# Performance work log

Measured on AMD Instinct MI355X. Metric: run time of the kernel, lower is better.

The kernel has to match this reference:

```python
import jax, jax.numpy as jnp
import numpy as np

EPS = 1e-5

def conv1x1(h, w, b):
    # h: [B,C,H,W], w: [O,C], b: [O]
    return jnp.einsum('bchw,oc->bohw', h, w) + b[None, :, None, None]

def setup_inputs() -> dict:
    key = jax.random.key(0)
    ks = jax.random.split(key, 10)
    B, C, H, W = 4, 256, 64, 64
    x = jax.random.normal(ks[0], (B, C, H, W), dtype=jnp.float32)
    s = 0.02
    return {
        'x': x,
        'gamma': jnp.ones((C,), jnp.float32),
        'beta': jnp.zeros((C,), jnp.float32),
        'wq': jax.random.normal(ks[1], (C, C), jnp.float32) * s,
        'bq': jnp.zeros((C,), jnp.float32),
        'wk': jax.random.normal(ks[2], (C, C), jnp.float32) * s,
        'bk': jnp.zeros((C,), jnp.float32),
        'wv': jax.random.normal(ks[3], (C, C), jnp.float32) * s,
        'bv': jnp.zeros((C,), jnp.float32),
        'wp': jax.random.normal(ks[4], (C, C), jnp.float32) * s,
        'bp': jnp.zeros((C,), jnp.float32),
    }

def reference(x, gamma, beta, wq, bq, wk, bk, wv, bv, wp, bp):
    B, C, H, W = x.shape
    N = H * W
    # BatchNorm2d (training mode: batch statistics, biased variance)
    mean = jnp.mean(x, axis=(0, 2, 3))
    var = jnp.var(x, axis=(0, 2, 3))
    h = (x - mean[None, :, None, None]) * jax.lax.rsqrt(var + EPS)[None, :, None, None]
    h = h * gamma[None, :, None, None] + beta[None, :, None, None]
    q = conv1x1(h, wq, bq).reshape(B, C, N)
    k = conv1x1(h, wk, bk).reshape(B, C, N)
    v = conv1x1(h, wv, bv).reshape(B, C, N)
    # scores[b,i,j] = q_i . k_j, softmax over j (keys)
    scores = jnp.einsum('bci,bcj->bij', q, k) * (C ** -0.5)
    attn = jax.nn.softmax(scores, axis=2)
    # out[b,c,i] = sum_j attn[b,i,j] * v[b,c,j]
    out = jnp.einsum('bij,bcj->bci', attn, v).reshape(B, C, H, W)
    out = conv1x1(out, wp, bp)
    return x + out
```

## Files before the change

kernel.cpp:

```cpp
#include <hip/hip_runtime.h>
#include <cstdint>
#include <cstddef>

#define B_ 4
#define C_ 256
#define N_ 4096

typedef __attribute__((ext_vector_type(8))) short s8v;
typedef __attribute__((ext_vector_type(4))) float f4v;
typedef __attribute__((ext_vector_type(16))) float f16v;

#if defined(__has_builtin)
#if __has_builtin(__builtin_amdgcn_exp2f)
#define EXP2(x) __builtin_amdgcn_exp2f(x)
#endif
#endif
#ifndef EXP2
#define EXP2(x) exp2f(x)
#endif

#define SCHED_FENCE() __builtin_amdgcn_sched_barrier(0)

__device__ __forceinline__ unsigned short f2bf(float f) {
  unsigned int u = __builtin_bit_cast(unsigned int, f);
  return (unsigned short)((u + 0x7FFFu + ((u >> 16) & 1u)) >> 16);
}

__device__ __forceinline__ unsigned pk2bf_trunc(float lo, float hi) {
  return __builtin_amdgcn_perm(__builtin_bit_cast(unsigned, hi),
                               __builtin_bit_cast(unsigned, lo), 0x07060302u);
}

__device__ __forceinline__ f16v zf16() {
  f16v z;
#pragma unroll
  for (int i = 0; i < 16; ++i) z[i] = 0.f;
  return z;
}


__global__ __launch_bounds__(256) void bn_stats(const float* __restrict__ x,
                                                float* __restrict__ mean,
                                                float* __restrict__ rstd) {
  int c = blockIdx.x, t = threadIdx.x;
  float s = 0.f, s2 = 0.f;
  for (int b = 0; b < B_; ++b) {
    const float* p = x + ((size_t)b * C_ + c) * N_;
    for (int n = t; n < N_; n += 256) { float v = p[n]; s += v; s2 += v * v; }
  }
  __shared__ float rs[256], rs2[256];
  rs[t] = s; rs2[t] = s2; __syncthreads();
  for (int off = 128; off > 0; off >>= 1) {
    if (t < off) { rs[t] += rs[t + off]; rs2[t] += rs2[t + off]; }
    __syncthreads();
  }
  if (t == 0) {
    float m = rs[0] * (1.f / 16384.f);
    float v = rs2[0] * (1.f / 16384.f) - m * m;
    mean[c] = m; rstd[c] = rsqrtf(v + 1e-5f);
  }
}

__global__ __launch_bounds__(256) void prep(
    const float* __restrict__ wq, const float* __restrict__ bq,
    const float* __restrict__ wk, const float* __restrict__ bk,
    const float* __restrict__ wv, const float* __restrict__ bv,
    const float* __restrict__ wp,
    const float* __restrict__ gamma, const float* __restrict__ beta,
    const float* __restrict__ mean, const float* __restrict__ rstd,
    unsigned short* __restrict__ wqb, unsigned short* __restrict__ wkb,
    unsigned short* __restrict__ wvb, unsigned short* __restrict__ wpb,
    float* __restrict__ beq, float* __restrict__ bek, float* __restrict__ bev) {
  const float QSC = 0.0625f * 1.4426950408889634f;
  int o = blockIdx.x, c = threadIdx.x;
  float a = gamma[c] * rstd[c];
  float d = beta[c] - mean[c] * a;
  float wqv = wq[o * C_ + c], wkv = wk[o * C_ + c], wvv = wv[o * C_ + c];
  wqb[o * C_ + c] = f2bf(wqv * a * QSC);
  wkb[o * C_ + c] = f2bf(wkv * a);
  wvb[o * C_ + c] = f2bf(wvv * a);
  wpb[o * C_ + c] = f2bf(wp[o * C_ + c]);
  __shared__ float r0[256], r1[256], r2[256];
  r0[c] = wqv * d; r1[c] = wkv * d; r2[c] = wvv * d; __syncthreads();
  for (int off = 128; off > 0; off >>= 1) {
    if (c < off) { r0[c] += r0[c + off]; r1[c] += r1[c + off]; r2[c] += r2[c + off]; }
    __syncthreads();
  }
  if (c == 0) {
    beq[o] = (bq[o] + r0[0]) * QSC;
    bek[o] = bk[o] + r1[0];
    bev[o] = bv[o] + r2[0];
  }
}

__global__ __launch_bounds__(256) void qkv(
    const float* __restrict__ x,
    const unsigned short* __restrict__ wqb, const unsigned short* __restrict__ wkb,
    const unsigned short* __restrict__ wvb,
    const float* __restrict__ beq, const float* __restrict__ bek,
    const float* __restrict__ bev,
    unsigned short* __restrict__ qB, unsigned short* __restrict__ kB,
    unsigned short* __restrict__ vB) {
  int b = blockIdx.z, oblk = blockIdx.y, n0 = blockIdx.x * 64;
  int tid = threadIdx.x, w = tid >> 6, l = tid & 63, quad = l >> 4, lq = l & 15;
  int orow = oblk * 64 + w * 16 + lq;

  __shared__ unsigned short XF[16384];
  __shared__ unsigned short Ls[64][72];

  {
    int cw = tid >> 6, nl = tid & 63;
    for (int cq = 0; cq < 4; ++cq) {
#pragma unroll
      for (int rr = 0; rr < 16; ++rr) {
        int c = cq * 64 + cw * 16 + rr;
        Ls[nl][cw * 16 + rr] = f2bf(x[((size_t)b * C_ + c) * N_ + n0 + nl]);
      }
      __syncthreads();
      int n_ = tid >> 2, cs = (tid & 3) * 16;
      s8v v0 = *(const s8v*)(&Ls[n_][cs]);
      s8v v1 = *(const s8v*)(&Ls[n_][cs + 8]);
      int fr = ((n_ >> 4) * 32 + ((cq * 64 + cs) >> 3)) * 128 + (n_ & 15) * 8;
      *(s8v*)(XF + fr) = v0;
      *(s8v*)(XF + fr + 128) = v1;
      __syncthreads();
    }
  }

  f4v aq[4], ak[4], av[4];
#pragma unroll
  for (int nt = 0; nt < 4; ++nt) {
    aq[nt] = (f4v){0.f, 0.f, 0.f, 0.f};
    ak[nt] = (f4v){0.f, 0.f, 0.f, 0.f};
    av[nt] = (f4v){0.f, 0.f, 0.f, 0.f};
  }

#pragma unroll
  for (int kk = 0; kk < 8; ++kk) {
    s8v afq = *(const s8v*)(wqb + (size_t)orow * C_ + kk * 32 + quad * 8);
    s8v afk = *(const s8v*)(wkb + (size_t)orow * C_ + kk * 32 + quad * 8);
    s8v afv = *(const s8v*)(wvb + (size_t)orow * C_ + kk * 32 + quad * 8);
#pragma unroll
    for (int nt = 0; nt < 4; ++nt) {
      s8v bf = *(const s8v*)(XF + (nt * 32 + kk * 4 + quad) * 128 + lq * 8);
      aq[nt] = __builtin_amdgcn_mfma_f32_16x16x32_bf16(afq, bf, aq[nt], 0, 0, 0);
      ak[nt] = __builtin_amdgcn_mfma_f32_16x16x32_bf16(afk, bf, ak[nt], 0, 0, 0);
      av[nt] = __builtin_amdgcn_mfma_f32_16x16x32_bf16(afv, bf, av[nt], 0, 0, 0);
    }
  }

  int obase = oblk * 64;

  for (int pass = 0; pass < 2; ++pass) {
    const f4v* acc = (pass == 0) ? aq : ak;
    const float* BE = (pass == 0) ? beq : bek;
    int ob4 = obase + w * 16 + quad * 4;
    float b0 = BE[ob4], b1 = BE[ob4 + 1], b2 = BE[ob4 + 2], b3 = BE[ob4 + 3];
    __syncthreads();
#pragma unroll
    for (int nt = 0; nt < 4; ++nt) {
      unsigned lo = (unsigned)f2bf(acc[nt][0] + b0) | ((unsigned)f2bf(acc[nt][1] + b1) << 16);
      unsigned hi = (unsigned)f2bf(acc[nt][2] + b2) | ((unsigned)f2bf(acc[nt][3] + b3) << 16);
      uint2 pr; pr.x = lo; pr.y = hi;
      *(uint2*)(&Ls[nt * 16 + lq][w * 16 + quad * 4]) = pr;
    }
    __syncthreads();
    {
      unsigned short* dp = (pass == 0) ? qB : kB;
#pragma unroll
      for (int ii = 0; ii < 2; ++ii) {
        int i = tid + ii * 256;
        int g = i >> 8, cs = (i >> 6) & 3, ll = i & 63;
        s8v vv = *(const s8v*)(&Ls[g * 32 + (ll & 31)][cs * 16 + ((ll >> 5) << 3)]);
        size_t dst;
        if (pass == 0)
          dst = ((((size_t)b * 64 + (n0 >> 6)) * 2 + g) * 16 + (obase >> 4) + cs) * 512 + (size_t)ll * 8;
        else
          dst = (((size_t)b * 128 + (n0 >> 5) + g) * 16 + (obase >> 4) + cs) * 512 + (size_t)ll * 8;
        *(s8v*)(dp + dst) = vv;
      }
    }
  }
  __syncthreads();

#pragma unroll
  for (int nt = 0; nt < 4; ++nt)
#pragma unroll
    for (int r = 0; r < 4; ++r) {
      int o_ = obase + w * 16 + quad * 4 + r;
      Ls[w * 16 + quad * 4 + r][nt * 16 + lq] = f2bf(av[nt][r] + bev[o_]);
    }
  __syncthreads();
  {
#pragma unroll
    for (int ii = 0; ii < 2; ++ii) {
      int i = tid + ii * 256;
      int g = i >> 8, ks = (i >> 6) & 3, ll = i & 63;
      s8v vv = *(const s8v*)(&Ls[g * 32 + (ll & 31)][ks * 16 + ((ll >> 5) << 3)]);
      size_t dst = (((size_t)b * 8 + (obase >> 5) + g) * 256 + (n0 >> 4) + ks) * 512 + (size_t)ll * 8;
      *(s8v*)(vB + dst) = vv;
    }
  }
}

__global__ __launch_bounds__(512, 2) void attn(
    const unsigned short* __restrict__ qB, const unsigned short* __restrict__ kB,
    const unsigned short* __restrict__ vB,
    const unsigned short* __restrict__ wpb, const float* __restrict__ bp,
    const float* __restrict__ x, float* __restrict__ out) {
  int id = blockIdx.x;
  int b = (id & 7) >> 1;
  int i0 = (((id >> 3) << 1) | (id & 1)) << 6;
  int tid = threadIdx.x, w = tid >> 6, l = tid & 63;
  int lh = l >> 5, l31 = l & 31;

  __shared__ unsigned short Qs[16384];
  __shared__ unsigned short Ps[2][16384];
  __shared__ unsigned short aS[16384];
  __shared__ float Lw[8][2][32];

  {
    const s8v* g = (const s8v*)(qB + ((size_t)b * 64 + (i0 >> 6)) * 16384);
    s8v* sq = (s8v*)Qs;
    sq[tid] = g[tid];
    sq[tid + 512] = g[tid + 512];
    sq[tid + 1024] = g[tid + 1024];
    sq[tid + 1536] = g[tid + 1536];
  }

  const unsigned short* kp = kB + (((size_t)b * 128 + w) * 16) * 512 + (size_t)l * 8;
  const unsigned short* vp = vB + (((size_t)b * 8 + w) * 256) * 512 + (size_t)l * 8;
  const unsigned short* Qp = Qs + (size_t)lh * 256 + l31 * 8;

  s8v kf[16];
#pragma unroll
  for (int cs = 0; cs < 16; ++cs) kf[cs] = *(const s8v*)(kp + cs * 512);
  SCHED_FENCE();

  __syncthreads();

  f16v O0 = zf16(), O1 = zf16();
  float ls0 = 0.f, ls1 = 0.f;

  for (int t = 0; t < 16; ++t) {
    s8v vf[16];
#pragma unroll
    for (int ks = 0; ks < 8; ++ks) vf[ks] = *(const s8v*)(vp + (size_t)ks * 512);
    SCHED_FENCE();
    f16v S0 = zf16(), S1 = zf16();
#pragma unroll
    for (int cs = 0; cs < 16; ++cs) {
      s8v q0 = *(const s8v*)(Qp + cs * 512);
      s8v q1 = *(const s8v*)(Qp + 8192 + cs * 512);
      S0 = __builtin_amdgcn_mfma_f32_32x32x16_bf16(kf[cs], q0, S0, 0, 0, 0);
      S1 = __builtin_amdgcn_mfma_f32_32x32x16_bf16(kf[cs], q1, S1, 0, 0, 0);
    }
#pragma unroll
    for (int ks = 8; ks < 16; ++ks) vf[ks] = *(const s8v*)(vp + (size_t)ks * 512);
    SCHED_FENCE();
    unsigned short* Pw = Ps[t & 1] + (w * 4) * 256 + l31 * 8 + lh * 4;
#pragma unroll
    for (int j = 0; j < 4; ++j) {
      float a0 = EXP2(S0[4 * j + 0]), a1 = EXP2(S0[4 * j + 1]);
      float a2 = EXP2(S0[4 * j + 2]), a3 = EXP2(S0[4 * j + 3]);
      ls0 += (a0 + a1) + (a2 + a3);
      uint2 p0; p0.x = pk2bf_trunc(a0, a1); p0.y = pk2bf_trunc(a2, a3);
      *(uint2*)(Pw + j * 256) = p0;
      float c0 = EXP2(S1[4 * j + 0]), c1 = EXP2(S1[4 * j + 1]);
      float c2 = EXP2(S1[4 * j + 2]), c3 = EXP2(S1[4 * j + 3]);
      ls1 += (c0 + c1) + (c2 + c3);
      uint2 p1; p1.x = pk2bf_trunc(c0, c1); p1.y = pk2bf_trunc(c2, c3);
      *(uint2*)(Pw + 8192 + j * 256) = p1;
    }
    __syncthreads();
    kp += 65536;
#pragma unroll
    for (int cs = 0; cs < 16; ++cs) kf[cs] = *(const s8v*)(kp + cs * 512);
    SCHED_FENCE();
    const unsigned short* Pr = Ps[t & 1] + (size_t)lh * 256 + l31 * 8;
#pragma unroll
    for (int ks = 0; ks < 16; ++ks) {
      s8v p0 = *(const s8v*)(Pr + ks * 512);
      s8v p1 = *(const s8v*)(Pr + ks * 512 + 8192);
      O0 = __builtin_amdgcn_mfma_f32_32x32x16_bf16(vf[ks], p0, O0, 0, 0, 0);
      O1 = __builtin_amdgcn_mfma_f32_32x32x16_bf16(vf[ks], p1, O1, 0, 0, 0);
    }
    vp += 8192;
  }

  s8v wf[16];
#pragma unroll
  for (int cs = 0; cs < 16; ++cs)
    wf[cs] = *(const s8v*)(wpb + (size_t)(w * 32 + l31) * 256 + cs * 16 + lh * 8);
  SCHED_FENCE();

  ls0 += __shfl_xor(ls0, 32);
  ls1 += __shfl_xor(ls1, 32);
  if (l < 32) { Lw[w][0][l] = ls0; Lw[w][1][l] = ls1; }
  __syncthreads();
  float s0 = 0.f, s1 = 0.f;
#pragma unroll
  for (int ww = 0; ww < 8; ++ww) { s0 += Lw[ww][0][l31]; s1 += Lw[ww][1][l31]; }
  float rl0 = 1.f / s0, rl1 = 1.f / s1;

#pragma unroll
  for (int jj = 0; jj < 4; ++jj) {
    ushort4 pk;
    pk.x = f2bf(O0[4 * jj + 0] * rl0); pk.y = f2bf(O0[4 * jj + 1] * rl0);
    pk.z = f2bf(O0[4 * jj + 2] * rl0); pk.w = f2bf(O0[4 * jj + 3] * rl0);
    int f0 = ((l31 >> 4) * 32 + w * 4 + jj) * 128 + (l31 & 15) * 8 + lh * 4;
    *(ushort4*)(aS + f0) = pk;
    pk.x = f2bf(O1[4 * jj + 0] * rl1); pk.y = f2bf(O1[4 * jj + 1] * rl1);
    pk.z = f2bf(O1[4 * jj + 2] * rl1); pk.w = f2bf(O1[4 * jj + 3] * rl1);
    int f1 = ((2 + (l31 >> 4)) * 32 + w * 4 + jj) * 128 + (l31 & 15) * 8 + lh * 4;
    *(ushort4*)(aS + f1) = pk;
  }
  __syncthreads();

  f16v OP0 = zf16(), OP1 = zf16();
#pragma unroll
  for (int cs = 0; cs < 16; ++cs) {
    s8v pa0 = *(const s8v*)(aS + ((0 + (l31 >> 4)) * 32 + cs * 2 + lh) * 128 + (l31 & 15) * 8);
    s8v pa1 = *(const s8v*)(aS + ((2 + (l31 >> 4)) * 32 + cs * 2 + lh) * 128 + (l31 & 15) * 8);
    OP0 = __builtin_amdgcn_mfma_f32_32x32x16_bf16(wf[cs], pa0, OP0, 0, 0, 0);
    OP1 = __builtin_amdgcn_mfma_f32_32x32x16_bf16(wf[cs], pa1, OP1, 0, 0, 0);
  }

#pragma unroll
  for (int r = 0; r < 16; ++r) {
    int o_ = w * 32 + (r & 3) + 8 * (r >> 2) + 4 * lh;
    float bpv = bp[o_];
    size_t ix = ((size_t)b * C_ + o_) * N_ + i0 + l31;
    out[ix]      = x[ix]      + OP0[r] + bpv;
    out[ix + 32] = x[ix + 32] + OP1[r] + bpv;
  }
}

extern "C" void kernel_launch(void* const* d_in, const int* in_sizes, int n_in,
                              void* d_out, int out_size, void* d_ws, size_t ws_size,
                              hipStream_t stream) {
  const float* x     = (const float*)d_in[0];
  const float* gamma = (const float*)d_in[1];
  const float* beta  = (const float*)d_in[2];
  const float* wq    = (const float*)d_in[3];
  const float* bq    = (const float*)d_in[4];
  const float* wk    = (const float*)d_in[5];
  const float* bk    = (const float*)d_in[6];
  const float* wv    = (const float*)d_in[7];
  const float* bv    = (const float*)d_in[8];
  const float* wp    = (const float*)d_in[9];
  const float* bp    = (const float*)d_in[10];
  float* out = (float*)d_out;

  char* ws = (char*)d_ws;
  float* mean = (float*)ws; ws += 1024;
  float* rstd = (float*)ws; ws += 1024;
  float* beq  = (float*)ws; ws += 1024;
  float* bek  = (float*)ws; ws += 1024;
  float* bev  = (float*)ws; ws += 1024;
  unsigned short* wqb = (unsigned short*)ws; ws += C_ * C_ * 2;
  unsigned short* wkb = (unsigned short*)ws; ws += C_ * C_ * 2;
  unsigned short* wvb = (unsigned short*)ws; ws += C_ * C_ * 2;
  unsigned short* wpb = (unsigned short*)ws; ws += C_ * C_ * 2;
  unsigned short* qB  = (unsigned short*)ws; ws += (size_t)B_ * N_ * C_ * 2;
  unsigned short* kB  = (unsigned short*)ws; ws += (size_t)B_ * N_ * C_ * 2;
  unsigned short* vB  = (unsigned short*)ws; ws += (size_t)B_ * N_ * C_ * 2;

  hipLaunchKernelGGL(bn_stats, dim3(C_), dim3(256), 0, stream, x, mean, rstd);
  hipLaunchKernelGGL(prep, dim3(C_), dim3(256), 0, stream,
                     wq, bq, wk, bk, wv, bv, wp, gamma, beta, mean, rstd,
                     wqb, wkb, wvb, wpb, beq, bek, bev);
  hipLaunchKernelGGL(qkv, dim3(N_ / 64, 4, B_), dim3(256), 0, stream,
                     x, wqb, wkb, wvb, beq, bek, bev, qB, kB, vB);
  hipLaunchKernelGGL(attn, dim3(256), dim3(512), 0, stream,
                     qB, kB, vB, wpb, bp, x, out);
}
```

Baseline: 206.5 us.

## Split attention waves into producer QK/softmax and consumer PV roles

Restructures the attention loop into warp specialization: waves 0-3 compute QK^T scores for two key groups each and write exp'd probabilities to a double-buffered LDS tile, while waves 4-7 consume the previous tile for the PV MFMA, one step behind. The projection staging buffer reuses the P buffer, freeing LDS. The goal is to overlap the exp/softmax phase with the PV matmul and cut the per-step sync count. Each wave now holds twice as many fragments, so register pressure rises, and the two roles may be unbalanced.

```diff
diff --git a/kernel.cpp b/kernel.cpp
--- a/kernel.cpp
+++ b/kernel.cpp
@@ -216,8 +216,7 @@
 
   __shared__ unsigned short Qs[16384];
   __shared__ unsigned short Ps[2][16384];
-  __shared__ unsigned short aS[16384];
-  __shared__ float Lw[8][2][32];
+  __shared__ float Lw[4][2][32];
 
   {
     const s8v* g = (const s8v*)(qB + ((size_t)b * 64 + (i0 >> 6)) * 16384);
@@ -228,64 +227,95 @@
     sq[tid + 1536] = g[tid + 1536];
   }
 
-  const unsigned short* kp = kB + (((size_t)b * 128 + w) * 16) * 512 + (size_t)l * 8;
-  const unsigned short* vp = vB + (((size_t)b * 8 + w) * 256) * 512 + (size_t)l * 8;
   const unsigned short* Qp = Qs + (size_t)lh * 256 + l31 * 8;
 
-  s8v kf[16];
-#pragma unroll
-  for (int cs = 0; cs < 16; ++cs) kf[cs] = *(const s8v*)(kp + cs * 512);
-  SCHED_FENCE();
+  const unsigned short* kp = kB + (((size_t)b * 128 + w * 2) * 16) * 512 + (size_t)l * 8;
+  const unsigned short* vp = vB + (((size_t)b * 8 + (w - 4) * 2) * 256) * 512 + (size_t)l * 8;
+
+  s8v kf[2][16];
+  s8v vf[2][16];
+  f16v O00 = zf16(), O01 = zf16(), O10 = zf16(), O11 = zf16();
+  float ls0 = 0.f, ls1 = 0.f;
+
+  if (w < 4) {
+#pragma unroll
+    for (int a = 0; a < 2; ++a)
+#pragma unroll
+      for (int cs = 0; cs < 16; ++cs) kf[a][cs] = *(const s8v*)(kp + (a * 16 + cs) * 512);
+    SCHED_FENCE();
+  }
 
   __syncthreads();
 
-  f16v O0 = zf16(), O1 = zf16();
-  float ls0 = 0.f, ls1 = 0.f;
-
-  for (int t = 0; t < 16; ++t) {
-    s8v vf[16];
-#pragma unroll
-    for (int ks = 0; ks < 8; ++ks) vf[ks] = *(const s8v*)(vp + (size_t)ks * 512);
-    SCHED_FENCE();
-    f16v S0 = zf16(), S1 = zf16();
-#pragma unroll
-    for (int cs = 0; cs < 16; ++cs) {
-      s8v q0 = *(const s8v*)(Qp + cs * 512);
-      s8v q1 = *(const s8v*)(Qp + 8192 + cs * 512);
-      S0 = __builtin_amdgcn_mfma_f32_32x32x16_bf16(kf[cs], q0, S0, 0, 0, 0);
-      S1 = __builtin_amdgcn_mfma_f32_32x32x16_bf16(kf[cs], q1, S1, 0, 0, 0);
-    }
-#pragma unroll
-    for (int ks = 8; ks < 16; ++ks) vf[ks] = *(const s8v*)(vp + (size_t)ks * 512);
-    SCHED_FENCE();
-    unsigned short* Pw = Ps[t & 1] + (w * 4) * 256 + l31 * 8 + lh * 4;
-#pragma unroll
-    for (int j = 0; j < 4; ++j) {
-      float a0 = EXP2(S0[4 * j + 0]), a1 = EXP2(S0[4 * j + 1]);
-      float a2 = EXP2(S0[4 * j + 2]), a3 = EXP2(S0[4 * j + 3]);
-      ls0 += (a0 + a1) + (a2 + a3);
-      uint2 p0; p0.x = pk2bf_trunc(a0, a1); p0.y = pk2bf_trunc(a2, a3);
-      *(uint2*)(Pw + j * 256) = p0;
-      float c0 = EXP2(S1[4 * j + 0]), c1 = EXP2(S1[4 * j + 1]);
-      float c2 = EXP2(S1[4 * j + 2]), c3 = EXP2(S1[4 * j + 3]);
-      ls1 += (c0 + c1) + (c2 + c3);
-      uint2 p1; p1.x = pk2bf_trunc(c0, c1); p1.y = pk2bf_trunc(c2, c3);
-      *(uint2*)(Pw + 8192 + j * 256) = p1;
+  for (int t = 0; t < 17; ++t) {
+    if (w < 4) {
+      if (t < 16) {
+        f16v S00 = zf16(), S01 = zf16(), S10 = zf16(), S11 = zf16();
+#pragma unroll
+        for (int cs = 0; cs < 16; ++cs) {
+          s8v q0 = *(const s8v*)(Qp + cs * 512);
+          s8v q1 = *(const s8v*)(Qp + 8192 + cs * 512);
+          S00 = __builtin_amdgcn_mfma_f32_32x32x16_bf16(kf[0][cs], q0, S00, 0, 0, 0);
+          S01 = __builtin_amdgcn_mfma_f32_32x32x16_bf16(kf[0][cs], q1, S01, 0, 0, 0);
+          S10 = __builtin_amdgcn_mfma_f32_32x32x16_bf16(kf[1][cs], q0, S10, 0, 0, 0);
+          S11 = __builtin_amdgcn_mfma_f32_32x32x16_bf16(kf[1][cs], q1, S11, 0, 0, 0);
+        }
+        SCHED_FENCE();
+        kp += 65536;
+#pragma unroll
+        for (int a = 0; a < 2; ++a)
+#pragma unroll
+          for (int cs = 0; cs < 16; ++cs) kf[a][cs] = *(const s8v*)(kp + (a * 16 + cs) * 512);
+        SCHED_FENCE();
+        unsigned short* Pb = Ps[t & 1] + (size_t)l31 * 8 + lh * 4;
+#pragma unroll
+        for (int a = 0; a < 2; ++a) {
+          const f16v& Sa0 = a ? S10 : S00;
+          const f16v& Sa1 = a ? S11 : S01;
+#pragma unroll
+          for (int j = 0; j < 4; ++j) {
+            int kg8 = w * 8 + a * 4 + j;
+            float e0 = EXP2(Sa0[4 * j + 0]), e1 = EXP2(Sa0[4 * j + 1]);
+            float e2 = EXP2(Sa0[4 * j + 2]), e3 = EXP2(Sa0[4 * j + 3]);
+            ls0 += (e0 + e1) + (e2 + e3);
+            uint2 p0; p0.x = pk2bf_trunc(e0, e1); p0.y = pk2bf_trunc(e2, e3);
+            *(uint2*)(Pb + kg8 * 256) = p0;
+            float c0 = EXP2(Sa1[4 * j + 0]), c1 = EXP2(Sa1[4 * j + 1]);
+            float c2 = EXP2(Sa1[4 * j + 2]), c3 = EXP2(Sa1[4 * j + 3]);
+            ls1 += (c0 + c1) + (c2 + c3);
+            uint2 p1; p1.x = pk2bf_trunc(c0, c1); p1.y = pk2bf_trunc(c2, c3);
+            *(uint2*)(Pb + kg8 * 256 + 8192) = p1;
+          }
+        }
+      } else {
+        ls0 += __shfl_xor(ls0, 32);
+        ls1 += __shfl_xor(ls1, 32);
+        if (l < 32) { Lw[w][0][l] = ls0; Lw[w][1][l] = ls1; }
+      }
+    } else {
+      if (t > 0) {
+        const unsigned short* Pr = Ps[(t - 1) & 1] + (size_t)lh * 256 + l31 * 8;
+#pragma unroll
+        for (int ks = 0; ks < 16; ++ks) {
+          s8v p0 = *(const s8v*)(Pr + ks * 512);
+          s8v p1 = *(const s8v*)(Pr + ks * 512 + 8192);
+          O00 = __builtin_amdgcn_mfma_f32_32x32x16_bf16(vf[0][ks], p0, O00, 0, 0, 0);
+          O01 = __builtin_amdgcn_mfma_f32_32x32x16_bf16(vf[0][ks], p1, O01, 0, 0, 0);
+          O10 = __builtin_amdgcn_mfma_f32_32x32x16_bf16(vf[1][ks], p0, O10, 0, 0, 0);
+          O11 = __builtin_amdgcn_mfma_f32_32x32x16_bf16(vf[1][ks], p1, O11, 0, 0, 0);
+        }
+      }
+      if (t < 16) {
+        SCHED_FENCE();
+#pragma unroll
+        for (int c = 0; c < 2; ++c)
+#pragma unroll
+          for (int ks = 0; ks < 16; ++ks)
+            vf[c][ks] = *(const s8v*)(vp + (size_t)c * 131072 + (size_t)(t * 16 + ks) * 512);
+        SCHED_FENCE();
+      }
     }
     __syncthreads();
-    kp += 65536;
-#pragma unroll
-    for (int cs = 0; cs < 16; ++cs) kf[cs] = *(const s8v*)(kp + cs * 512);
-    SCHED_FENCE();
-    const unsigned short* Pr = Ps[t & 1] + (size_t)lh * 256 + l31 * 8;
-#pragma unroll
-    for (int ks = 0; ks < 16; ++ks) {
-      s8v p0 = *(const s8v*)(Pr + ks * 512);
-      s8v p1 = *(const s8v*)(Pr + ks * 512 + 8192);
-      O0 = __builtin_amdgcn_mfma_f32_32x32x16_bf16(vf[ks], p0, O0, 0, 0, 0);
-      O1 = __builtin_amdgcn_mfma_f32_32x32x16_bf16(vf[ks], p1, O1, 0, 0, 0);
-    }
-    vp += 8192;
   }
 
   s8v wf[16];
@@ -294,26 +324,30 @@
     wf[cs] = *(const s8v*)(wpb + (size_t)(w * 32 + l31) * 256 + cs * 16 + lh * 8);
   SCHED_FENCE();
 
-  ls0 += __shfl_xor(ls0, 32);
-  ls1 += __shfl_xor(ls1, 32);
-  if (l < 32) { Lw[w][0][l] = ls0; Lw[w][1][l] = ls1; }
-  __syncthreads();
-  float s0 = 0.f, s1 = 0.f;
-#pragma unroll
-  for (int ww = 0; ww < 8; ++ww) { s0 += Lw[ww][0][l31]; s1 += Lw[ww][1][l31]; }
-  float rl0 = 1.f / s0, rl1 = 1.f / s1;
-
-#pragma unroll
-  for (int jj = 0; jj < 4; ++jj) {
-    ushort4 pk;
-    pk.x = f2bf(O0[4 * jj + 0] * rl0); pk.y = f2bf(O0[4 * jj + 1] * rl0);
-    pk.z = f2bf(O0[4 * jj + 2] * rl0); pk.w = f2bf(O0[4 * jj + 3] * rl0);
-    int f0 = ((l31 >> 4) * 32 + w * 4 + jj) * 128 + (l31 & 15) * 8 + lh * 4;
-    *(ushort4*)(aS + f0) = pk;
-    pk.x = f2bf(O1[4 * jj + 0] * rl1); pk.y = f2bf(O1[4 * jj + 1] * rl1);
-    pk.z = f2bf(O1[4 * jj + 2] * rl1); pk.w = f2bf(O1[4 * jj + 3] * rl1);
-    int f1 = ((2 + (l31 >> 4)) * 32 + w * 4 + jj) * 128 + (l31 & 15) * 8 + lh * 4;
-    *(ushort4*)(aS + f1) = pk;
+  unsigned short* aS = Ps[0];
+  if (w >= 4) {
+    int pw = w - 4;
+    float s0 = Lw[0][0][l31] + Lw[1][0][l31] + Lw[2][0][l31] + Lw[3][0][l31];
+    float s1 = Lw[0][1][l31] + Lw[1][1][l31] + Lw[2][1][l31] + Lw[3][1][l31];
+    float rl0 = 1.f / s0, rl1 = 1.f / s1;
+#pragma unroll
+    for (int cg = 0; cg < 2; ++cg) {
+      const f16v& Or0 = cg ? O10 : O00;
+      const f16v& Or1 = cg ? O11 : O01;
+#pragma unroll
+      for (int jj = 0; jj < 4; ++jj) {
+        int cb = pw * 8 + cg * 4 + jj;
+        ushort4 pk;
+        pk.x = f2bf(Or0[4 * jj + 0] * rl0); pk.y = f2bf(Or0[4 * jj + 1] * rl0);
+        pk.z = f2bf(Or0[4 * jj + 2] * rl0); pk.w = f2bf(Or0[4 * jj + 3] * rl0);
+        int f0 = (((l31 >> 4)) * 32 + cb) * 128 + (l31 & 15) * 8 + lh * 4;
+        *(ushort4*)(aS + f0) = pk;
+        pk.x = f2bf(Or1[4 * jj + 0] * rl1); pk.y = f2bf(Or1[4 * jj + 1] * rl1);
+        pk.z = f2bf(Or1[4 * jj + 2] * rl1); pk.w = f2bf(Or1[4 * jj + 3] * rl1);
+        int f1 = ((2 + (l31 >> 4)) * 32 + cb) * 128 + (l31 & 15) * 8 + lh * 4;
+        *(ushort4*)(aS + f1) = pk;
+      }
+    }
   }
   __syncthreads();
 
```

Result: slower. 477.0 us (+131.0%).

## Software-pipeline attention loop: overlap QK^T of next tile with PV of previous

Applied to the files above, without the earlier changes.

Restructures the attention main loop into a skewed 17-iteration pipeline. Each iteration interleaves the QK^T MFMAs for tile t with the PV MFMAs for tile t-1, which reads P from the other buffer, and there is one barrier per iteration instead of one mid-loop. The V and K fragments for the next tile are loaded together before the exp/packing phase. Keeping both kf and vf live raises register pressure, so launch bounds drop to one block per CU (512 threads), trading occupancy for intra-wave overlap.

```diff
diff --git a/kernel.cpp b/kernel.cpp
--- a/kernel.cpp
+++ b/kernel.cpp
@@ -203,7 +203,7 @@
   }
 }
 
-__global__ __launch_bounds__(512, 2) void attn(
+__global__ __launch_bounds__(512, 1) void attn(
     const unsigned short* __restrict__ qB, const unsigned short* __restrict__ kB,
     const unsigned short* __restrict__ vB,
     const unsigned short* __restrict__ wpb, const float* __restrict__ bp,
@@ -239,53 +239,69 @@
 
   __syncthreads();
 
+  s8v vf[16];
   f16v O0 = zf16(), O1 = zf16();
   float ls0 = 0.f, ls1 = 0.f;
 
-  for (int t = 0; t < 16; ++t) {
-    s8v vf[16];
-#pragma unroll
-    for (int ks = 0; ks < 8; ++ks) vf[ks] = *(const s8v*)(vp + (size_t)ks * 512);
-    SCHED_FENCE();
+  for (int t = 0; t < 17; ++t) {
     f16v S0 = zf16(), S1 = zf16();
-#pragma unroll
-    for (int cs = 0; cs < 16; ++cs) {
-      s8v q0 = *(const s8v*)(Qp + cs * 512);
-      s8v q1 = *(const s8v*)(Qp + 8192 + cs * 512);
-      S0 = __builtin_amdgcn_mfma_f32_32x32x16_bf16(kf[cs], q0, S0, 0, 0, 0);
-      S1 = __builtin_amdgcn_mfma_f32_32x32x16_bf16(kf[cs], q1, S1, 0, 0, 0);
-    }
-#pragma unroll
-    for (int ks = 8; ks < 16; ++ks) vf[ks] = *(const s8v*)(vp + (size_t)ks * 512);
-    SCHED_FENCE();
-    unsigned short* Pw = Ps[t & 1] + (w * 4) * 256 + l31 * 8 + lh * 4;
-#pragma unroll
-    for (int j = 0; j < 4; ++j) {
-      float a0 = EXP2(S0[4 * j + 0]), a1 = EXP2(S0[4 * j + 1]);
-      float a2 = EXP2(S0[4 * j + 2]), a3 = EXP2(S0[4 * j + 3]);
-      ls0 += (a0 + a1) + (a2 + a3);
-      uint2 p0; p0.x = pk2bf_trunc(a0, a1); p0.y = pk2bf_trunc(a2, a3);
-      *(uint2*)(Pw + j * 256) = p0;
-      float c0 = EXP2(S1[4 * j + 0]), c1 = EXP2(S1[4 * j + 1]);
-      float c2 = EXP2(S1[4 * j + 2]), c3 = EXP2(S1[4 * j + 3]);
-      ls1 += (c0 + c1) + (c2 + c3);
-      uint2 p1; p1.x = pk2bf_trunc(c0, c1); p1.y = pk2bf_trunc(c2, c3);
-      *(uint2*)(Pw + 8192 + j * 256) = p1;
-    }
-    __syncthreads();
-    kp += 65536;
-#pragma unroll
-    for (int cs = 0; cs < 16; ++cs) kf[cs] = *(const s8v*)(kp + cs * 512);
-    SCHED_FENCE();
-    const unsigned short* Pr = Ps[t & 1] + (size_t)lh * 256 + l31 * 8;
-#pragma unroll
-    for (int ks = 0; ks < 16; ++ks) {
-      s8v p0 = *(const s8v*)(Pr + ks * 512);
-      s8v p1 = *(const s8v*)(Pr + ks * 512 + 8192);
-      O0 = __builtin_amdgcn_mfma_f32_32x32x16_bf16(vf[ks], p0, O0, 0, 0, 0);
-      O1 = __builtin_amdgcn_mfma_f32_32x32x16_bf16(vf[ks], p1, O1, 0, 0, 0);
-    }
-    vp += 8192;
+    const unsigned short* Pr = Ps[(t + 1) & 1] + (size_t)lh * 256 + l31 * 8;
+
+    if (t == 0) {
+#pragma unroll
+      for (int i = 0; i < 16; ++i) {
+        s8v q0 = *(const s8v*)(Qp + i * 512);
+        s8v q1 = *(const s8v*)(Qp + 8192 + i * 512);
+        S0 = __builtin_amdgcn_mfma_f32_32x32x16_bf16(kf[i], q0, S0, 0, 0, 0);
+        S1 = __builtin_amdgcn_mfma_f32_32x32x16_bf16(kf[i], q1, S1, 0, 0, 0);
+      }
+    } else if (t < 16) {
+#pragma unroll
+      for (int i = 0; i < 16; ++i) {
+        s8v q0 = *(const s8v*)(Qp + i * 512);
+        s8v q1 = *(const s8v*)(Qp + 8192 + i * 512);
+        s8v p0 = *(const s8v*)(Pr + i * 512);
+        s8v p1 = *(const s8v*)(Pr + i * 512 + 8192);
+        S0 = __builtin_amdgcn_mfma_f32_32x32x16_bf16(kf[i], q0, S0, 0, 0, 0);
+        O0 = __builtin_amdgcn_mfma_f32_32x32x16_bf16(vf[i], p0, O0, 0, 0, 0);
+        S1 = __builtin_amdgcn_mfma_f32_32x32x16_bf16(kf[i], q1, S1, 0, 0, 0);
+        O1 = __builtin_amdgcn_mfma_f32_32x32x16_bf16(vf[i], p1, O1, 0, 0, 0);
+      }
+    } else {
+#pragma unroll
+      for (int i = 0; i < 16; ++i) {
+        s8v p0 = *(const s8v*)(Pr + i * 512);
+        s8v p1 = *(const s8v*)(Pr + i * 512 + 8192);
+        O0 = __builtin_amdgcn_mfma_f32_32x32x16_bf16(vf[i], p0, O0, 0, 0, 0);
+        O1 = __builtin_amdgcn_mfma_f32_32x32x16_bf16(vf[i], p1, O1, 0, 0, 0);
+      }
+    }
+
+    if (t < 16) {
+      SCHED_FENCE();
+#pragma unroll
+      for (int ks = 0; ks < 16; ++ks) vf[ks] = *(const s8v*)(vp + (size_t)ks * 512);
+      vp += 8192;
+      kp += 65536;
+#pragma unroll
+      for (int cs = 0; cs < 16; ++cs) kf[cs] = *(const s8v*)(kp + cs * 512);
+      SCHED_FENCE();
+      unsigned short* Pw = Ps[t & 1] + (w * 4) * 256 + l31 * 8 + lh * 4;
+#pragma unroll
+      for (int j = 0; j < 4; ++j) {
+        float a0 = EXP2(S0[4 * j + 0]), a1 = EXP2(S0[4 * j + 1]);
+        float a2 = EXP2(S0[4 * j + 2]), a3 = EXP2(S0[4 * j + 3]);
+        ls0 += (a0 + a1) + (a2 + a3);
+        uint2 p0; p0.x = pk2bf_trunc(a0, a1); p0.y = pk2bf_trunc(a2, a3);
+        *(uint2*)(Pw + j * 256) = p0;
+        float c0 = EXP2(S1[4 * j + 0]), c1 = EXP2(S1[4 * j + 1]);
+        float c2 = EXP2(S1[4 * j + 2]), c3 = EXP2(S1[4 * j + 3]);
+        ls1 += (c0 + c1) + (c2 + c3);
+        uint2 p1; p1.x = pk2bf_trunc(c0, c1); p1.y = pk2bf_trunc(c2, c3);
+        *(uint2*)(Pw + 8192 + j * 256) = p1;
+      }
+    }
+    __syncthreads();
   }
 
   s8v wf[16];
```

After: 205.6 us. Within noise of the previous version (-0.5%).

## Use FP8 for V and P in the attention PV matmul

Applied to the files above, without the earlier changes.

V is now stored as FP8 (converted from bf16 in the qkv kernel) and the softmax probabilities P are packed to FP8 in LDS, so the PV product uses the fp8 MFMA instruction. This halves V global traffic, the V register footprint and the P shared-memory traffic. It also loads all V fragments up front and raises wave priority around the MFMA loops with s_setprio. The cost is reduced precision in the attention output, which may hurt accuracy.

```diff
diff --git a/kernel.cpp b/kernel.cpp
--- a/kernel.cpp
+++ b/kernel.cpp
@@ -9,6 +9,7 @@
 typedef __attribute__((ext_vector_type(8))) short s8v;
 typedef __attribute__((ext_vector_type(4))) float f4v;
 typedef __attribute__((ext_vector_type(16))) float f16v;
+typedef long long i64f;
 
 #if defined(__has_builtin)
 #if __has_builtin(__builtin_amdgcn_exp2f)
@@ -26,9 +27,8 @@
   return (unsigned short)((u + 0x7FFFu + ((u >> 16) & 1u)) >> 16);
 }
 
-__device__ __forceinline__ unsigned pk2bf_trunc(float lo, float hi) {
-  return __builtin_amdgcn_perm(__builtin_bit_cast(unsigned, hi),
-                               __builtin_bit_cast(unsigned, lo), 0x07060302u);
+__device__ __forceinline__ float bf2f(unsigned short u) {
+  return __builtin_bit_cast(float, (unsigned)u << 16);
 }
 
 __device__ __forceinline__ f16v zf16() {
@@ -100,7 +100,7 @@
     const float* __restrict__ beq, const float* __restrict__ bek,
     const float* __restrict__ bev,
     unsigned short* __restrict__ qB, unsigned short* __restrict__ kB,
-    unsigned short* __restrict__ vB) {
+    unsigned char* __restrict__ vB) {
   int b = blockIdx.z, oblk = blockIdx.y, n0 = blockIdx.x * 64;
   int tid = threadIdx.x, w = tid >> 6, l = tid & 63, quad = l >> 4, lq = l & 15;
   int orow = oblk * 64 + w * 16 + lq;
@@ -197,15 +197,24 @@
       int i = tid + ii * 256;
       int g = i >> 8, ks = (i >> 6) & 3, ll = i & 63;
       s8v vv = *(const s8v*)(&Ls[g * 32 + (ll & 31)][ks * 16 + ((ll >> 5) << 3)]);
-      size_t dst = (((size_t)b * 8 + (obase >> 5) + g) * 256 + (n0 >> 4) + ks) * 512 + (size_t)ll * 8;
-      *(s8v*)(vB + dst) = vv;
+      unsigned w0 = (unsigned)__builtin_amdgcn_cvt_pk_fp8_f32(
+          bf2f((unsigned short)vv[0]), bf2f((unsigned short)vv[1]), 0, false);
+      w0 = (unsigned)__builtin_amdgcn_cvt_pk_fp8_f32(
+          bf2f((unsigned short)vv[2]), bf2f((unsigned short)vv[3]), (int)w0, true);
+      unsigned w1 = (unsigned)__builtin_amdgcn_cvt_pk_fp8_f32(
+          bf2f((unsigned short)vv[4]), bf2f((unsigned short)vv[5]), 0, false);
+      w1 = (unsigned)__builtin_amdgcn_cvt_pk_fp8_f32(
+          bf2f((unsigned short)vv[6]), bf2f((unsigned short)vv[7]), (int)w1, true);
+      uint2 pr; pr.x = w0; pr.y = w1;
+      size_t dst = ((((size_t)b * 8 + (obase >> 5) + g) * 256 + (n0 >> 4) + ks) * 64 + ll) * 8;
+      *(uint2*)(vB + dst) = pr;
     }
   }
 }
 
 __global__ __launch_bounds__(512, 2) void attn(
     const unsigned short* __restrict__ qB, const unsigned short* __restrict__ kB,
-    const unsigned short* __restrict__ vB,
+    const unsigned char* __restrict__ vB,
     const unsigned short* __restrict__ wpb, const float* __restrict__ bp,
     const float* __restrict__ x, float* __restrict__ out) {
   int id = blockIdx.x;
@@ -215,7 +224,7 @@
   int lh = l >> 5, l31 = l & 31;
 
   __shared__ unsigned short Qs[16384];
-  __shared__ unsigned short Ps[2][16384];
+  __shared__ unsigned char Ps[2][16384];
   __shared__ unsigned short aS[16384];
   __shared__ float Lw[8][2][32];
 
@@ -229,7 +238,7 @@
   }
 
   const unsigned short* kp = kB + (((size_t)b * 128 + w) * 16) * 512 + (size_t)l * 8;
-  const unsigned short* vp = vB + (((size_t)b * 8 + w) * 256) * 512 + (size_t)l * 8;
+  const unsigned char* vp = vB + (((size_t)b * 8 + w) * 256) * 512 + (size_t)l * 8;
   const unsigned short* Qp = Qs + (size_t)lh * 256 + l31 * 8;
 
   s8v kf[16];
@@ -243,11 +252,12 @@
   float ls0 = 0.f, ls1 = 0.f;
 
   for (int t = 0; t < 16; ++t) {
-    s8v vf[16];
-#pragma unroll
-    for (int ks = 0; ks < 8; ++ks) vf[ks] = *(const s8v*)(vp + (size_t)ks * 512);
+    i64f vf[16];
+#pragma unroll
+    for (int ks = 0; ks < 16; ++ks) vf[ks] = *(const i64f*)(vp + ks * 512);
     SCHED_FENCE();
     f16v S0 = zf16(), S1 = zf16();
+    __builtin_amdgcn_s_setprio(1);
 #pragma unroll
     for (int cs = 0; cs < 16; ++cs) {
       s8v q0 = *(const s8v*)(Qp + cs * 512);
@@ -255,36 +265,39 @@
       S0 = __builtin_amdgcn_mfma_f32_32x32x16_bf16(kf[cs], q0, S0, 0, 0, 0);
       S1 = __builtin_amdgcn_mfma_f32_32x32x16_bf16(kf[cs], q1, S1, 0, 0, 0);
     }
-#pragma unroll
-    for (int ks = 8; ks < 16; ++ks) vf[ks] = *(const s8v*)(vp + (size_t)ks * 512);
+    __builtin_amdgcn_s_setprio(0);
     SCHED_FENCE();
-    unsigned short* Pw = Ps[t & 1] + (w * 4) * 256 + l31 * 8 + lh * 4;
+    unsigned char* Pw = Ps[t & 1] + (w * 4) * 512 + l31 * 8 + lh * 4;
 #pragma unroll
     for (int j = 0; j < 4; ++j) {
       float a0 = EXP2(S0[4 * j + 0]), a1 = EXP2(S0[4 * j + 1]);
       float a2 = EXP2(S0[4 * j + 2]), a3 = EXP2(S0[4 * j + 3]);
       ls0 += (a0 + a1) + (a2 + a3);
-      uint2 p0; p0.x = pk2bf_trunc(a0, a1); p0.y = pk2bf_trunc(a2, a3);
-      *(uint2*)(Pw + j * 256) = p0;
+      unsigned p0 = (unsigned)__builtin_amdgcn_cvt_pk_fp8_f32(a0, a1, 0, false);
+      p0 = (unsigned)__builtin_amdgcn_cvt_pk_fp8_f32(a2, a3, (int)p0, true);
+      *(unsigned*)(Pw + j * 512) = p0;
       float c0 = EXP2(S1[4 * j + 0]), c1 = EXP2(S1[4 * j + 1]);
       float c2 = EXP2(S1[4 * j + 2]), c3 = EXP2(S1[4 * j + 3]);
       ls1 += (c0 + c1) + (c2 + c3);
-      uint2 p1; p1.x = pk2bf_trunc(c0, c1); p1.y = pk2bf_trunc(c2, c3);
-      *(uint2*)(Pw + 8192 + j * 256) = p1;
+      unsigned p1 = (unsigned)__builtin_amdgcn_cvt_pk_fp8_f32(c0, c1, 0, false);
+      p1 = (unsigned)__builtin_amdgcn_cvt_pk_fp8_f32(c2, c3, (int)p1, true);
+      *(unsigned*)(Pw + j * 512 + 256) = p1;
     }
     __syncthreads();
     kp += 65536;
 #pragma unroll
     for (int cs = 0; cs < 16; ++cs) kf[cs] = *(const s8v*)(kp + cs * 512);
     SCHED_FENCE();
-    const unsigned short* Pr = Ps[t & 1] + (size_t)lh * 256 + l31 * 8;
+    const unsigned char* Pr = Ps[t & 1] + (size_t)lh * 512 + l31 * 8;
+    __builtin_amdgcn_s_setprio(1);
 #pragma unroll
     for (int ks = 0; ks < 16; ++ks) {
-      s8v p0 = *(const s8v*)(Pr + ks * 512);
-      s8v p1 = *(const s8v*)(Pr + ks * 512 + 8192);
-      O0 = __builtin_amdgcn_mfma_f32_32x32x16_bf16(vf[ks], p0, O0, 0, 0, 0);
-      O1 = __builtin_amdgcn_mfma_f32_32x32x16_bf16(vf[ks], p1, O1, 0, 0, 0);
-    }
+      i64f p0 = *(const i64f*)(Pr + ks * 1024);
+      i64f p1 = *(const i64f*)(Pr + ks * 1024 + 256);
+      O0 = __builtin_amdgcn_mfma_f32_32x32x16_fp8_fp8(vf[ks], p0, O0, 0, 0, 0);
+      O1 = __builtin_amdgcn_mfma_f32_32x32x16_fp8_fp8(vf[ks], p1, O1, 0, 0, 0);
+    }
+    __builtin_amdgcn_s_setprio(0);
     vp += 8192;
   }
 
@@ -364,7 +377,7 @@
   unsigned short* wpb = (unsigned short*)ws; ws += C_ * C_ * 2;
   unsigned short* qB  = (unsigned short*)ws; ws += (size_t)B_ * N_ * C_ * 2;
   unsigned short* kB  = (unsigned short*)ws; ws += (size_t)B_ * N_ * C_ * 2;
-  unsigned short* vB  = (unsigned short*)ws; ws += (size_t)B_ * N_ * C_ * 2;
+  unsigned char*  vB  = (unsigned char*)ws;  ws += (size_t)B_ * N_ * C_ * 2;
 
   hipLaunchKernelGGL(bn_stats, dim3(C_), dim3(256), 0, stream, x, mean, rstd);
   hipLaunchKernelGGL(prep, dim3(C_), dim3(256), 0, stream,
```

After: 199.6 us. -3.4%, faster.
